# Performance work log

Hardware: AMD Instinct MI355X
Metric: run time of the kernel (lower is better)

## Reference

```python
import jax, jax.numpy as jnp
import numpy as np

B, N, F_IN, H, C = 4, 2048, 128, 4, 32
NEG_SLOPE = 0.2
EDGE_DENSITY = 0.01  # ~20 avg degree


def setup_inputs() -> dict:
    key = jax.random.key(0)
    ks = jax.random.split(key, 6)
    x = jax.random.normal(ks[0], (B, N, F_IN), dtype=jnp.float32)
    adj = (jax.random.uniform(ks[1], (B, N, N)) < EDGE_DENSITY).astype(jnp.float32)
    # glorot-style scaled params
    W = jax.random.normal(ks[2], (F_IN, H * C), dtype=jnp.float32) * (2.0 / (F_IN + H * C)) ** 0.5
    att_src = jax.random.normal(ks[3], (H, C), dtype=jnp.float32) * (2.0 / (1 + C)) ** 0.5
    att_dst = jax.random.normal(ks[4], (H, C), dtype=jnp.float32) * (2.0 / (1 + C)) ** 0.5
    bias = jnp.zeros((H * C,), dtype=jnp.float32)
    return {"x": x, "adj": adj, "W": W, "att_src": att_src, "att_dst": att_dst, "bias": bias}


def reference(x, adj, W, att_src, att_dst, bias):
    b, n, _ = x.shape
    h, c = att_src.shape
    # add self-loops
    idx = jnp.arange(n)
    adj = adj.at[:, idx, idx].set(1.0)
    # linear projection: [B,N,H,C]
    out = (x @ W).reshape(b, n, h, c)
    a_src = jnp.einsum('bnhc,hc->bnh', out, att_src)
    a_dst = jnp.einsum('bnhc,hc->bnh', out, att_dst)
    # alpha[b,i,j,h] = a_src[b,i,h] + a_dst[b,j,h]  -> [B,N,N,H]
    alpha = a_src[:, :, None, :] + a_dst[:, None, :, :]
    alpha = jax.nn.leaky_relu(alpha, NEG_SLOPE)
    alpha = adj[..., None] * jnp.exp(alpha)
    # faithful to original: normalize over dim=1 (the i axis)
    alpha = alpha / alpha.sum(axis=1, keepdims=True)
    # out_i = sum_j alpha[b,i,j,h] * feat[b,j,h,c]
    o = jnp.einsum('bijh,bjhc->bihc', alpha, out)
    o = o.reshape(b, n, h * c) + bias
    return o
```

## Files before the change

kernel.cpp:

```cpp
#include <hip/hip_runtime.h>
#include <math.h>

#define BB 4
#define NN 2048
#define F_IN 128
#define HH 4
#define CC 32
#define HC 128
#define NEG_SLOPE 0.2f
#define CAP 64
#define RT 256
#define CT 128
#define NRT 8
#define NCT 16
#define LCAP 768

__device__ __forceinline__ float lrelu(float v) {
    return v > 0.f ? v : NEG_SLOPE * v;
}

__global__ __launch_bounds__(256) void k_gemm_att(const float* __restrict__ x,
                                                  const float* __restrict__ W,
                                                  const float* __restrict__ att_src,
                                                  const float* __restrict__ att_dst,
                                                  float* __restrict__ feat,
                                                  float* __restrict__ a_src,
                                                  float* __restrict__ a_dst,
                                                  int* __restrict__ cnt) {
    __shared__ float xs[32][F_IN];
    __shared__ float fs[32][HC + 1];
    const long row0 = (long)blockIdx.x * 32;
    const int t = threadIdx.x;
    for (int idx = t; idx < 32 * F_IN; idx += 256)
        xs[idx >> 7][idx & 127] = x[row0 * F_IN + idx];
    __syncthreads();
    const int col = t & 127;
    const int rg  = t >> 7;
    float acc[16];
#pragma unroll
    for (int r = 0; r < 16; ++r) acc[r] = 0.f;
    for (int k = 0; k < F_IN; ++k) {
        float w = W[k * HC + col];
#pragma unroll
        for (int r = 0; r < 16; ++r)
            acc[r] += xs[rg + 2 * r][k] * w;
    }
#pragma unroll
    for (int r = 0; r < 16; ++r) {
        feat[(row0 + rg + 2 * r) * HC + col] = acc[r];
        fs[rg + 2 * r][col] = acc[r];
    }
    __syncthreads();
    if (t < 128) {
        const int row = t & 31;
        const int h   = t >> 5;
        float s = 0.f, d = 0.f;
#pragma unroll
        for (int c = 0; c < CC; ++c) {
            float v = fs[row][h * CC + c];
            s += v * att_src[h * CC + c];
            d += v * att_dst[h * CC + c];
        }
        a_src[(row0 + row) * 4 + h] = s;
        a_dst[(row0 + row) * 4 + h] = d;
    }
    if (t < 32) cnt[blockIdx.x * 32 + t] = 0;
}

__global__ __launch_bounds__(256) void k_tile(const float4* __restrict__ adj4,
                                              const float4* __restrict__ as4g,
                                              const float4* __restrict__ ad4g,
                                              int* __restrict__ cnt,
                                              unsigned short* __restrict__ nbr,
                                              float4* __restrict__ partial) {
    const int bx = blockIdx.x;
    const int b  = bx >> 7;
    const int rt = (bx >> 4) & 7;
    const int ct = bx & 15;
    const int i0 = rt * RT;
    const int c0 = ct * CT;
    const int t  = threadIdx.x;

    __shared__ float4 as4[RT];
    __shared__ float4 ad4[CT];
    __shared__ float4 pd[CT];
    __shared__ unsigned short blist[LCAP];
    __shared__ int rowcnt[RT];
    __shared__ int rowoff[RT];
    __shared__ int nent;

    as4[t] = as4g[(b << 11) + i0 + t];
    if (t < CT) {
        ad4[t] = ad4g[(b << 11) + c0 + t];
        pd[t] = make_float4(0.f, 0.f, 0.f, 0.f);
    }
    rowcnt[t] = 0;
    if (t == 0) nent = 0;
    __syncthreads();

    const float4* base = adj4 + ((long)((b << 11) + i0)) * (NN / 4) + (c0 >> 2);
    int idx0 = t * 4;
    float4 v = base[(idx0 >> 7) * (NN / 4) + ((idx0 & 127) >> 2)];
    for (int s = 0; s < 32; ++s) {
        const int idx = s * 1024 + t * 4;
        const float4 cur = v;
        if (s < 31) {
            const int nx = idx + 1024;
            v = base[(nx >> 7) * (NN / 4) + ((nx & 127) >> 2)];
        }
        const int il = idx >> 7;
        const int j0 = idx & 127;
        const int gi = i0 + il;
#pragma unroll
        for (int k = 0; k < 4; ++k) {
            const float vv = (&cur.x)[k];
            if (vv != 0.f || gi == c0 + j0 + k) {
                int pos = atomicAdd(&nent, 1);
                if (pos < LCAP) blist[pos] = (unsigned short)((il << 7) | (j0 + k));
                atomicAdd(&rowcnt[il], 1);
            }
        }
    }
    __syncthreads();

    {
        int rc = rowcnt[t];
        int bs = 0;
        if (rc > 0) bs = atomicAdd(&cnt[(b << 11) + i0 + t], rc);
        rowoff[t] = bs;
    }
    __syncthreads();

    const int ne = min(nent, LCAP);
    for (int e = t; e < ne; e += 256) {
        const int pk = blist[e];
        const int il = pk >> 7;
        const int jl = pk & 127;
        const float4 s4 = as4[il];
        const float4 d4 = ad4[jl];
        atomicAdd(&(&pd[jl].x)[0], __expf(lrelu(s4.x + d4.x)));
        atomicAdd(&(&pd[jl].x)[1], __expf(lrelu(s4.y + d4.y)));
        atomicAdd(&(&pd[jl].x)[2], __expf(lrelu(s4.z + d4.z)));
        atomicAdd(&(&pd[jl].x)[3], __expf(lrelu(s4.w + d4.w)));
        int slot = atomicAdd(&rowoff[il], 1);
        if (slot < CAP)
            nbr[((long)((b << 11) + i0 + il)) * CAP + slot] = (unsigned short)(c0 + jl);
    }
    __syncthreads();

    if (t < CT)
        partial[((long)(b * NRT + rt) << 11) + c0 + t] = pd[t];
}

__global__ __launch_bounds__(256) void k_rdenom(const float4* __restrict__ partial,
                                                float4* __restrict__ rdenom) {
    const int u = blockIdx.x * blockDim.x + threadIdx.x;
    if (u >= BB * NN) return;
    const int b = u >> 11;
    const int j = u & 2047;
    float4 s = make_float4(0.f, 0.f, 0.f, 0.f);
#pragma unroll
    for (int rt = 0; rt < NRT; ++rt) {
        float4 p = partial[((long)(b * NRT + rt) << 11) + j];
        s.x += p.x; s.y += p.y; s.z += p.z; s.w += p.w;
    }
    rdenom[u] = make_float4(1.f / s.x, 1.f / s.y, 1.f / s.z, 1.f / s.w);
}

__global__ __launch_bounds__(128) void k_aggr(const float* __restrict__ feat,
                                              const float* __restrict__ a_src,
                                              const float4* __restrict__ ad4,
                                              const float4* __restrict__ rd4,
                                              const int* __restrict__ cnt,
                                              const unsigned short* __restrict__ nbr,
                                              const float* __restrict__ bias,
                                              float* __restrict__ out) {
    const int bi = blockIdx.x;
    const int b  = bi >> 11;
    const int t  = threadIdx.x;
    __shared__ float4 s_coef[CAP];
    __shared__ int    s_j[CAP];
    __shared__ float  s_as[4];
    const int n = min(cnt[bi], CAP);
    if (t < 4) s_as[t] = a_src[bi * 4 + t];
    if (t < n) s_j[t] = nbr[(long)bi * CAP + t];
    __syncthreads();
    if (t < n) {
        const int j = s_j[t];
        const float4 ad = ad4[(b << 11) + j];
        const float4 rd = rd4[(b << 11) + j];
        float4 c;
        c.x = __expf(lrelu(s_as[0] + ad.x)) * rd.x;
        c.y = __expf(lrelu(s_as[1] + ad.y)) * rd.y;
        c.z = __expf(lrelu(s_as[2] + ad.z)) * rd.z;
        c.w = __expf(lrelu(s_as[3] + ad.w)) * rd.w;
        s_coef[t] = c;
    }
    __syncthreads();
    const int h = t >> 5;
    const float* fb = feat + ((long)(b << 11)) * HC + t;
    float a0 = 0.f, a1 = 0.f, a2 = 0.f, a3 = 0.f;
    int s = 0;
    for (; s + 4 <= n; s += 4) {
        int j0 = s_j[s + 0], j1 = s_j[s + 1], j2 = s_j[s + 2], j3 = s_j[s + 3];
        float c0 = (&s_coef[s + 0].x)[h], c1 = (&s_coef[s + 1].x)[h];
        float c2 = (&s_coef[s + 2].x)[h], c3 = (&s_coef[s + 3].x)[h];
        a0 += c0 * fb[(long)j0 * HC];
        a1 += c1 * fb[(long)j1 * HC];
        a2 += c2 * fb[(long)j2 * HC];
        a3 += c3 * fb[(long)j3 * HC];
    }
    for (; s < n; ++s)
        a0 += (&s_coef[s].x)[h] * fb[(long)s_j[s] * HC];
    out[(long)bi * HC + t] = (a0 + a1) + (a2 + a3) + bias[t];
}

extern "C" void kernel_launch(void* const* d_in, const int* in_sizes, int n_in,
                              void* d_out, int out_size, void* d_ws, size_t ws_size,
                              hipStream_t stream) {
    const float* x       = (const float*)d_in[0];
    const float* adj     = (const float*)d_in[1];
    const float* W       = (const float*)d_in[2];
    const float* att_src = (const float*)d_in[3];
    const float* att_dst = (const float*)d_in[4];
    const float* bias    = (const float*)d_in[5];
    float* out = (float*)d_out;

    float* feat    = (float*)d_ws;
    float* a_src   = feat    + (long)BB * NN * HC;
    float* a_dst   = a_src   + (long)BB * NN * HH;
    float* rdenom  = a_dst   + (long)BB * NN * HH;
    float* partial = rdenom  + (long)BB * NN * HH;
    int*   cnt     = (int*)(partial + (long)BB * NRT * NN * HH);
    unsigned short* nbr = (unsigned short*)(cnt + (long)BB * NN);

    k_gemm_att<<<(BB * NN) / 32, 256, 0, stream>>>(x, W, att_src, att_dst,
                                                   feat, a_src, a_dst, cnt);
    k_tile<<<BB * NRT * NCT, 256, 0, stream>>>((const float4*)adj, (const float4*)a_src,
                                               (const float4*)a_dst, cnt, nbr,
                                               (float4*)partial);
    k_rdenom<<<(BB * NN + 255) / 256, 256, 0, stream>>>((const float4*)partial,
                                                        (float4*)rdenom);
    k_aggr<<<BB * NN, 128, 0, stream>>>(feat, a_src, (const float4*)a_dst,
                                        (const float4*)rdenom, cnt, nbr, bias, out);
}
```

Before: 148.1 us.

## Shrink adjacency row tiles to 64 and deepen gather unrolling

Reduces the row tile of the adjacency scan kernel from 256 to 64 rows, which quadruples the number of blocks and shrinks the per-block edge list capacity. The scan is restructured so each warp reads a contiguous row segment with two loads in flight at a time. The aggregation kernel's neighbor gather is unrolled to 8 independent accumulators to expose more memory-level parallelism. The aim is more parallelism and latency hiding on the bandwidth-bound adjacency read, at the cost of more partial-denominator tiles and more global atomics.

New measurement: 142.4 us. -3.9%, faster.

```diff
diff --git a/kernel.cpp b/kernel.cpp
--- a/kernel.cpp
+++ b/kernel.cpp
@@ -9,11 +9,11 @@
 #define HC 128
 #define NEG_SLOPE 0.2f
 #define CAP 64
-#define RT 256
+#define RT 64
 #define CT 128
-#define NRT 8
+#define NRT 32
 #define NCT 16
-#define LCAP 768
+#define LCAP 320
 
 __device__ __forceinline__ float lrelu(float v) {
     return v > 0.f ? v : NEG_SLOPE * v;
@@ -74,8 +74,8 @@
                                               unsigned short* __restrict__ nbr,
                                               float4* __restrict__ partial) {
     const int bx = blockIdx.x;
-    const int b  = bx >> 7;
-    const int rt = (bx >> 4) & 7;
+    const int b  = bx >> 9;
+    const int rt = (bx >> 4) & 31;
     const int ct = bx & 15;
     const int i0 = rt * RT;
     const int c0 = ct * CT;
@@ -89,41 +89,52 @@
     __shared__ int rowoff[RT];
     __shared__ int nent;
 
-    as4[t] = as4g[(b << 11) + i0 + t];
+    if (t < RT) {
+        as4[t] = as4g[(b << 11) + i0 + t];
+        rowcnt[t] = 0;
+    }
     if (t < CT) {
         ad4[t] = ad4g[(b << 11) + c0 + t];
         pd[t] = make_float4(0.f, 0.f, 0.f, 0.f);
     }
-    rowcnt[t] = 0;
     if (t == 0) nent = 0;
     __syncthreads();
 
-    const float4* base = adj4 + ((long)((b << 11) + i0)) * (NN / 4) + (c0 >> 2);
-    int idx0 = t * 4;
-    float4 v = base[(idx0 >> 7) * (NN / 4) + ((idx0 & 127) >> 2)];
-    for (int s = 0; s < 32; ++s) {
-        const int idx = s * 1024 + t * 4;
-        const float4 cur = v;
-        if (s < 31) {
-            const int nx = idx + 1024;
-            v = base[(nx >> 7) * (NN / 4) + ((nx & 127) >> 2)];
-        }
-        const int il = idx >> 7;
-        const int j0 = idx & 127;
-        const int gi = i0 + il;
-#pragma unroll
-        for (int k = 0; k < 4; ++k) {
-            const float vv = (&cur.x)[k];
-            if (vv != 0.f || gi == c0 + j0 + k) {
-                int pos = atomicAdd(&nent, 1);
-                if (pos < LCAP) blist[pos] = (unsigned short)((il << 7) | (j0 + k));
-                atomicAdd(&rowcnt[il], 1);
-            }
-        }
-    }
-    __syncthreads();
-
-    {
+    const float4* p = adj4 + ((long)((b << 11) + i0) + (t >> 5)) * (NN / 4)
+                    + (c0 >> 2) + (t & 31);
+    const int jb = (t & 31) * 4;
+    const int rl = t >> 5;
+
+#define PROCESS(V, S)                                                          \
+    {                                                                          \
+        const int il = (S) * 8 + rl;                                           \
+        const int gi = i0 + il;                                                \
+        _Pragma("unroll")                                                      \
+        for (int k = 0; k < 4; ++k) {                                          \
+            const float vv = (&(V).x)[k];                                      \
+            if (vv != 0.f || gi == c0 + jb + k) {                              \
+                int pos = atomicAdd(&nent, 1);                                 \
+                if (pos < LCAP)                                                \
+                    blist[pos] = (unsigned short)((il << 7) | (jb + k));       \
+                atomicAdd(&rowcnt[il], 1);                                     \
+            }                                                                  \
+        }                                                                      \
+    }
+
+    float4 v0 = p[0];
+    float4 v1 = p[8 * (NN / 4)];
+    for (int s = 0; s < 8; s += 2) {
+        const float4 c0v = v0;
+        const float4 c1v = v1;
+        if (s + 2 < 8) v0 = p[(s + 2) * 8 * (NN / 4)];
+        if (s + 3 < 8) v1 = p[(s + 3) * 8 * (NN / 4)];
+        PROCESS(c0v, s)
+        PROCESS(c1v, s + 1)
+    }
+#undef PROCESS
+    __syncthreads();
+
+    if (t < RT) {
         int rc = rowcnt[t];
         int bs = 0;
         if (rc > 0) bs = atomicAdd(&cnt[(b << 11) + i0 + t], rc);
@@ -200,19 +211,23 @@
     const int h = t >> 5;
     const float* fb = feat + ((long)(b << 11)) * HC + t;
     float a0 = 0.f, a1 = 0.f, a2 = 0.f, a3 = 0.f;
+    float a4 = 0.f, a5 = 0.f, a6 = 0.f, a7 = 0.f;
     int s = 0;
-    for (; s + 4 <= n; s += 4) {
+    for (; s + 8 <= n; s += 8) {
         int j0 = s_j[s + 0], j1 = s_j[s + 1], j2 = s_j[s + 2], j3 = s_j[s + 3];
-        float c0 = (&s_coef[s + 0].x)[h], c1 = (&s_coef[s + 1].x)[h];
-        float c2 = (&s_coef[s + 2].x)[h], c3 = (&s_coef[s + 3].x)[h];
-        a0 += c0 * fb[(long)j0 * HC];
-        a1 += c1 * fb[(long)j1 * HC];
-        a2 += c2 * fb[(long)j2 * HC];
-        a3 += c3 * fb[(long)j3 * HC];
+        int j4 = s_j[s + 4], j5 = s_j[s + 5], j6 = s_j[s + 6], j7 = s_j[s + 7];
+        a0 += (&s_coef[s + 0].x)[h] * fb[(long)j0 * HC];
+        a1 += (&s_coef[s + 1].x)[h] * fb[(long)j1 * HC];
+        a2 += (&s_coef[s + 2].x)[h] * fb[(long)j2 * HC];
+        a3 += (&s_coef[s + 3].x)[h] * fb[(long)j3 * HC];
+        a4 += (&s_coef[s + 4].x)[h] * fb[(long)j4 * HC];
+        a5 += (&s_coef[s + 5].x)[h] * fb[(long)j5 * HC];
+        a6 += (&s_coef[s + 6].x)[h] * fb[(long)j6 * HC];
+        a7 += (&s_coef[s + 7].x)[h] * fb[(long)j7 * HC];
     }
     for (; s < n; ++s)
         a0 += (&s_coef[s].x)[h] * fb[(long)s_j[s] * HC];
-    out[(long)bi * HC + t] = (a0 + a1) + (a2 + a3) + bias[t];
+    out[(long)bi * HC + t] = ((a0 + a1) + (a2 + a3)) + ((a4 + a5) + (a6 + a7)) + bias[t];
 }
 
 extern "C" void kernel_launch(void* const* d_in, const int* in_sizes, int n_in,
```
